# Optimization experiments

Hardware: AMD Instinct MI355X
Metric: run time of the kernel (lower is better)

## Reference

```python
import jax, jax.numpy as jnp
import numpy as np


def setup_inputs() -> dict:
    key = jax.random.key(0)
    ks = jax.random.split(key, 8)
    B = 65536
    x = jax.random.normal(ks[0], (B, 784), dtype=jnp.float32)
    conv_w = jnp.ones((3, 3), dtype=jnp.float32)  # Parameter(ones((3,3)))
    # Linear layers stored as (in, out) weight + (out,) bias
    def lin(k, fin, fout):
        kw, kb = jax.random.split(k)
        bound = 1.0 / np.sqrt(fin)
        W = jax.random.uniform(kw, (fin, fout), minval=-bound, maxval=bound, dtype=jnp.float32)
        b = jax.random.uniform(kb, (fout,), minval=-bound, maxval=bound, dtype=jnp.float32)
        return W, b
    W1, b1 = lin(ks[1], 26 * 26, 500)
    W2, b2 = lin(ks[2], 500, 200)
    W3, b3 = lin(ks[3], 200, 10)
    return {"x": x, "conv_w": conv_w, "W1": W1, "b1": b1,
            "W2": W2, "b2": b2, "W3": W3, "b3": b3}


def reference(x, conv_w, W1, b1, W2, b2, W3, b3):
    B = x.shape[0]
    img = x.reshape(B, 1, 28, 28)  # NCHW, single channel
    kern = conv_w.reshape(1, 1, 3, 3)  # OIHW
    # valid 2D cross-correlation == torch tensordot sliding-window loop
    conv = jax.lax.conv_general_dilated(
        img, kern, window_strides=(1, 1), padding='VALID',
        dimension_numbers=('NCHW', 'OIHW', 'NCHW'))  # (B,1,26,26)
    h = conv.reshape(B, 26 * 26)
    h = jax.nn.relu(h @ W1 + b1)
    h = jax.nn.relu(h @ W2 + b2)
    return h @ W3 + b3  # (B, 10) logits
```

## Files before the change

### kernel.cpp

```cpp
#include <hip/hip_runtime.h>
#include <hip/hip_bf16.h>
#include <stdint.h>

typedef __bf16 bf16x8 __attribute__((ext_vector_type(8)));
typedef float  f32x4  __attribute__((ext_vector_type(4)));


#define KT1 25
#define NF1 32
#define KT2 16
#define NF2 16
#define KT3 8

__global__ void prep_w1(const float* __restrict__ W1, const float* __restrict__ cw,
                        __bf16* __restrict__ w1s) {
  int gid  = blockIdx.x * 256 + threadIdx.x;
  int lane = gid & 63;
  int slot = gid >> 6;
  int t = slot >> 5;
  int f = slot & 31;
  int kbase = t * 32 + ((lane >> 4) << 3);
  int n = f * 16 + (lane & 15);
  float c[9];
#pragma unroll
  for (int i = 0; i < 9; ++i) c[i] = cw[i];
  bf16x8 v;
#pragma unroll
  for (int e = 0; e < 8; ++e) {
    int k = kbase + e;
    float acc = 0.f;
    if (k < 784 && n < 500) {
      int pi = k / 28, pj = k % 28;
#pragma unroll
      for (int dr = 0; dr < 3; ++dr) {
        int r = pi - dr;
        if (r < 0 || r >= 26) continue;
#pragma unroll
        for (int dc = 0; dc < 3; ++dc) {
          int cc = pj - dc;
          if (cc < 0 || cc >= 26) continue;
          acc += c[dr * 3 + dc] * W1[(size_t)(r * 26 + cc) * 500 + n];
        }
      }
    }
    v[e] = (__bf16)acc;
  }
  *(bf16x8*)(w1s + (size_t)(slot * 64 + lane) * 8) = v;
}

__global__ void prep_w2(const float* __restrict__ W2, __bf16* __restrict__ w2s) {
  int gid  = blockIdx.x * 256 + threadIdx.x;
  int lane = gid & 63;
  int slot = gid >> 6;
  int t = slot >> 4;
  int f = slot & 15;
  int kbase = t * 32 + ((lane >> 4) << 3);
  int n = f * 16 + (lane & 15);
  bf16x8 v;
#pragma unroll
  for (int e = 0; e < 8; ++e) {
    int k = kbase + e;
    float val = (k < 500 && n < 200) ? W2[(size_t)k * 200 + n] : 0.f;
    v[e] = (__bf16)val;
  }
  *(bf16x8*)(w2s + (size_t)(slot * 64 + lane) * 8) = v;
}

__global__ void prep_w3(const float* __restrict__ W3, __bf16* __restrict__ w3s) {
  int gid  = blockIdx.x * 256 + threadIdx.x;
  int lane = gid & 63;
  int t    = gid >> 6;
  int kbase = t * 32 + ((lane >> 4) << 3);
  int n = lane & 15;
  bf16x8 v;
#pragma unroll
  for (int e = 0; e < 8; ++e) {
    int k = kbase + e;
    float val = (k < 200 && n < 10) ? W3[(size_t)k * 10 + n] : 0.f;
    v[e] = (__bf16)val;
  }
  *(bf16x8*)(w3s + (size_t)(t * 64 + lane) * 8) = v;
}

__global__ __launch_bounds__(256, 2) void mlp_fused(
    const float* __restrict__ x,
    const __bf16* __restrict__ w1s, const __bf16* __restrict__ w2s,
    const __bf16* __restrict__ w3s,
    const float* __restrict__ b1, const float* __restrict__ b2,
    const float* __restrict__ b3,
    float* __restrict__ out)
{
  __shared__ __align__(16) char xsm[2 * 4096];
  __shared__ __align__(16) char h1[64 * 1024];
  __shared__ float sb1[512];
  __shared__ float sb2[256];

  const int tid  = threadIdx.x;
  const int lane = tid & 63;
  const int w    = tid >> 6;
  const int lrow = lane & 15;
  const int lgrp = lane >> 4;
  const int brow = blockIdx.x * 64;
  const int xr   = tid >> 2;
  const int xq   = tid & 3;

  sb1[tid]       = (tid < 500) ? b1[tid] : 0.f;
  sb1[tid + 256] = (tid + 256 < 500) ? b1[tid + 256] : 0.f;
  sb2[tid]       = (tid < 200) ? b2[tid] : 0.f;

  const f32x4 FZ = {0.f, 0.f, 0.f, 0.f};

  f32x4 acc1[4][8];
#pragma unroll
  for (int m = 0; m < 4; ++m)
#pragma unroll
    for (int f = 0; f < 8; ++f) acc1[m][f] = FZ;

  const bf16x8* w1p   = (const bf16x8*)w1s + ((size_t)(w * 8) * 64 + lane);
  const float*  xbase = x + (size_t)(brow + xr) * 784;
  const int     xswz  = (xq ^ (xr & 3)) << 4;
  const int     xoff  = xr * 64 + xswz;

  auto gload = [&](int t, f32x4 (&g)[2]) {
    int gk = t * 32 + xq * 8;
    if (gk > 776) gk = 776;
    const float* p = xbase + gk;
    g[0] = *(const f32x4*)p;
    g[1] = *(const f32x4*)(p + 4);
  };
  auto cwrite = [&](f32x4 (&g)[2], int bw) {
    bf16x8 v;
#pragma unroll
    for (int e = 0; e < 4; ++e) { v[e] = (__bf16)g[0][e]; v[e + 4] = (__bf16)g[1][e]; }
    *(bf16x8*)(xsm + bw + xoff) = v;
  };

  f32x4  grA[2], grB[2];
  bf16x8 bA[8], bB[8];

  auto body1 = [&](int t, bf16x8 (&bc)[8], bf16x8 (&bn)[8],
                   f32x4 (&gc)[2], f32x4 (&gl)[2], int bufR, int bufW) {
    bf16x8 afr[4];
#pragma unroll
    for (int m = 0; m < 4; ++m) {
      int r = m * 16 + lrow;
      afr[m] = *(const bf16x8*)(xsm + bufR + r * 64 + ((lgrp ^ (r & 3)) << 4));
    }
#pragma unroll
    for (int f = 0; f < 8; ++f) bn[f] = w1p[(size_t)((t + 1) * NF1 + f) * 64];
    gload(t + 2 > 24 ? 24 : t + 2, gl);
    cwrite(gc, bufW);

    __builtin_amdgcn_s_setprio(1);
#pragma unroll
    for (int f = 0; f < 8; ++f)
#pragma unroll
      for (int m = 0; m < 4; ++m)
        acc1[m][f] = __builtin_amdgcn_mfma_f32_16x16x32_bf16(afr[m], bc[f], acc1[m][f], 0, 0, 0);
    __builtin_amdgcn_s_setprio(0);

    asm volatile("s_waitcnt lgkmcnt(0)\n\ts_barrier" ::: "memory");
  };

  gload(0, grA);
#pragma unroll
  for (int f = 0; f < 8; ++f) bA[f] = w1p[(size_t)f * 64];
  gload(1, grB);
  cwrite(grA, 0);
  asm volatile("s_waitcnt lgkmcnt(0)\n\ts_barrier" ::: "memory");

  for (int t = 0; t < 24; t += 2) {
    body1(t,     bA, bB, grB, grA, 0,    4096);
    body1(t + 1, bB, bA, grA, grB, 4096, 0);
  }
  {
    bf16x8 afr[4];
#pragma unroll
    for (int m = 0; m < 4; ++m) {
      int r = m * 16 + lrow;
      afr[m] = *(const bf16x8*)(xsm + r * 64 + ((lgrp ^ (r & 3)) << 4));
    }
    __builtin_amdgcn_s_setprio(1);
#pragma unroll
    for (int f = 0; f < 8; ++f)
#pragma unroll
      for (int m = 0; m < 4; ++m)
        acc1[m][f] = __builtin_amdgcn_mfma_f32_16x16x32_bf16(afr[m], bA[f], acc1[m][f], 0, 0, 0);
    __builtin_amdgcn_s_setprio(0);
  }

#pragma unroll
  for (int m = 0; m < 4; ++m) {
#pragma unroll
    for (int f = 0; f < 8; ++f) {
      int col = w * 128 + f * 16 + lrow;
      float bias = sb1[col];
#pragma unroll
      for (int r = 0; r < 4; ++r) {
        int row = m * 16 + lgrp * 4 + r;
        float v = fmaxf(acc1[m][f][r] + bias, 0.f);
        int off = row * 1024 + ((col * 2) ^ ((row & 7) << 4));
        *(__bf16*)(h1 + off) = (__bf16)v;
      }
    }
  }
  __syncthreads();

  f32x4 acc2[4][4];
#pragma unroll
  for (int m = 0; m < 4; ++m)
#pragma unroll
    for (int f = 0; f < 4; ++f) acc2[m][f] = FZ;

  const bf16x8* w2p = (const bf16x8*)w2s + ((size_t)(w * 4) * 64 + lane);

  bf16x8 b2a[4], b2b[4];
#pragma unroll
  for (int f = 0; f < 4; ++f) b2a[f] = w2p[(size_t)f * 64];

  for (int t = 0; t < KT2; t += 2) {
#pragma unroll
    for (int f = 0; f < 4; ++f) b2b[f] = w2p[(size_t)((t + 1) * NF2 + f) * 64];
    {
      bf16x8 a2[4];
#pragma unroll
      for (int m = 0; m < 4; ++m) {
        int row = m * 16 + lrow;
        int off = row * 1024 + ((t * 64 + lgrp * 16) ^ ((row & 7) << 4));
        a2[m] = *(const bf16x8*)(h1 + off);
      }
      __builtin_amdgcn_s_setprio(1);
#pragma unroll
      for (int f = 0; f < 4; ++f)
#pragma unroll
        for (int m = 0; m < 4; ++m)
          acc2[m][f] = __builtin_amdgcn_mfma_f32_16x16x32_bf16(a2[m], b2a[f], acc2[m][f], 0, 0, 0);
      __builtin_amdgcn_s_setprio(0);
    }
#pragma unroll
    for (int f = 0; f < 4; ++f) b2a[f] = w2p[(size_t)((t + 2) * NF2 + f) * 64];
    {
      bf16x8 a2[4];
#pragma unroll
      for (int m = 0; m < 4; ++m) {
        int row = m * 16 + lrow;
        int off = row * 1024 + (((t + 1) * 64 + lgrp * 16) ^ ((row & 7) << 4));
        a2[m] = *(const bf16x8*)(h1 + off);
      }
      __builtin_amdgcn_s_setprio(1);
#pragma unroll
      for (int f = 0; f < 4; ++f)
#pragma unroll
        for (int m = 0; m < 4; ++m)
          acc2[m][f] = __builtin_amdgcn_mfma_f32_16x16x32_bf16(a2[m], b2b[f], acc2[m][f], 0, 0, 0);
      __builtin_amdgcn_s_setprio(0);
    }
  }

  __syncthreads();

#pragma unroll
  for (int m = 0; m < 4; ++m) {
#pragma unroll
    for (int f = 0; f < 4; ++f) {
      int col = w * 64 + f * 16 + lrow;
      float bias = sb2[col];
#pragma unroll
      for (int r = 0; r < 4; ++r) {
        int row = m * 16 + lgrp * 4 + r;
        float v = fmaxf(acc2[m][f][r] + bias, 0.f);
        int off = row * 512 + ((col * 2) ^ ((row & 7) << 4));
        *(__bf16*)(h1 + off) = (__bf16)v;
      }
    }
  }
  __syncthreads();

  {
    f32x4 a3 = FZ;
    const bf16x8* w3p = (const bf16x8*)w3s + lane;
#pragma unroll
    for (int t = 0; t < KT3; ++t) {
      int row = w * 16 + lrow;
      int off = row * 512 + ((t * 64 + lgrp * 16) ^ ((row & 7) << 4));
      bf16x8 a = *(const bf16x8*)(h1 + off);
      a3 = __builtin_amdgcn_mfma_f32_16x16x32_bf16(a, w3p[(size_t)t * 64], a3, 0, 0, 0);
    }
    if (lrow < 10) {
      float bias = b3[lrow];
#pragma unroll
      for (int r = 0; r < 4; ++r)
        out[(size_t)(brow + w * 16 + lgrp * 4 + r) * 10 + lrow] = a3[r] + bias;
    }
  }
}

extern "C" void kernel_launch(void* const* d_in, const int* in_sizes, int n_in,
                              void* d_out, int out_size, void* d_ws, size_t ws_size,
                              hipStream_t stream) {
  const float* x  = (const float*)d_in[0];
  const float* cw = (const float*)d_in[1];
  const float* W1 = (const float*)d_in[2];
  const float* b1 = (const float*)d_in[3];
  const float* W2 = (const float*)d_in[4];
  const float* b2 = (const float*)d_in[5];
  const float* W3 = (const float*)d_in[6];
  const float* b3 = (const float*)d_in[7];
  float* out = (float*)d_out;

  __bf16* w1s = (__bf16*)d_ws;
  __bf16* w2s = w1s + (size_t)KT1 * NF1 * 64 * 8;
  __bf16* w3s = w2s + (size_t)KT2 * NF2 * 64 * 8;

  prep_w1<<<200, 256, 0, stream>>>(W1, cw, w1s);
  prep_w2<<<64, 256, 0, stream>>>(W2, w2s);
  prep_w3<<<2, 256, 0, stream>>>(W3, w3s);

  mlp_fused<<<65536 / 64, 256, 0, stream>>>(x, w1s, w2s, w3s, b1, b2, b3, out);
}
```

Baseline: 93.04 us.

## Stage four x K-tiles per barrier and alias x buffer with h1 LDS

Restructures the layer-1 pipeline so each stage loads four 32-wide K-tiles of x into registers, writes them as a 16KB bf16 LDS block, and double-buffers those blocks. A barrier is now needed only once per four tiles instead of once per tile, which cuts synchronisation cost and gives each global load more time to arrive. The x staging buffer is aliased onto the h1 activation buffer, so total LDS use drops from 72KB to 64KB plus biases. The cost is more registers holding in-flight loads, which may hurt occupancy at launch bounds of 2 blocks. The W2 prefetch is also moved ahead of the layer-1 epilogue.

```diff
diff --git a/kernel.cpp b/kernel.cpp
--- a/kernel.cpp
+++ b/kernel.cpp
@@ -90,8 +90,7 @@
     const float* __restrict__ b3,
     float* __restrict__ out)
 {
-  __shared__ __align__(16) char xsm[2 * 4096];
-  __shared__ __align__(16) char h1[64 * 1024];
+  __shared__ __align__(16) char smem[64 * 1024];
   __shared__ float sb1[512];
   __shared__ float sb2[256];
 
@@ -118,39 +117,45 @@
 
   const bf16x8* w1p   = (const bf16x8*)w1s + ((size_t)(w * 8) * 64 + lane);
   const float*  xbase = x + (size_t)(brow + xr) * 784;
-  const int     xswz  = (xq ^ (xr & 3)) << 4;
-  const int     xoff  = xr * 64 + xswz;
-
-  auto gload = [&](int t, f32x4 (&g)[2]) {
-    int gk = t * 32 + xq * 8;
-    if (gk > 776) gk = 776;
-    const float* p = xbase + gk;
-    g[0] = *(const f32x4*)p;
-    g[1] = *(const f32x4*)(p + 4);
+  const int     xoff  = xr * 64 + ((xq ^ (xr & 3)) << 4);
+
+  f32x4 g[4][2];
+
+  auto gload4 = [&](int s) {
+#pragma unroll
+    for (int j = 0; j < 4; ++j) {
+      int tile = s * 4 + j;
+      if (tile > 24) tile = 24;
+      int gk = tile * 32 + xq * 8;
+      if (gk > 776) gk = 776;
+      const float* p = xbase + gk;
+      g[j][0] = *(const f32x4*)p;
+      g[j][1] = *(const f32x4*)(p + 4);
+    }
   };
-  auto cwrite = [&](f32x4 (&g)[2], int bw) {
-    bf16x8 v;
-#pragma unroll
-    for (int e = 0; e < 4; ++e) { v[e] = (__bf16)g[0][e]; v[e + 4] = (__bf16)g[1][e]; }
-    *(bf16x8*)(xsm + bw + xoff) = v;
+  auto cwrite4 = [&](int buf) {
+#pragma unroll
+    for (int j = 0; j < 4; ++j) {
+      bf16x8 v;
+#pragma unroll
+      for (int e = 0; e < 4; ++e) { v[e] = (__bf16)g[j][0][e]; v[e + 4] = (__bf16)g[j][1][e]; }
+      *(bf16x8*)(smem + buf * 16384 + j * 4096 + xoff) = v;
+    }
   };
 
-  f32x4  grA[2], grB[2];
   bf16x8 bA[8], bB[8];
 
-  auto body1 = [&](int t, bf16x8 (&bc)[8], bf16x8 (&bn)[8],
-                   f32x4 (&gc)[2], f32x4 (&gl)[2], int bufR, int bufW) {
+  auto ktile = [&](int tile, int rb, int slot, bf16x8 (&bc)[8], bf16x8 (&bn)[8], bool pf) {
     bf16x8 afr[4];
 #pragma unroll
     for (int m = 0; m < 4; ++m) {
       int r = m * 16 + lrow;
-      afr[m] = *(const bf16x8*)(xsm + bufR + r * 64 + ((lgrp ^ (r & 3)) << 4));
-    }
-#pragma unroll
-    for (int f = 0; f < 8; ++f) bn[f] = w1p[(size_t)((t + 1) * NF1 + f) * 64];
-    gload(t + 2 > 24 ? 24 : t + 2, gl);
-    cwrite(gc, bufW);
-
+      afr[m] = *(const bf16x8*)(smem + rb + slot * 4096 + r * 64 + ((lgrp ^ (r & 3)) << 4));
+    }
+    if (pf) {
+#pragma unroll
+      for (int f = 0; f < 8; ++f) bn[f] = w1p[(size_t)((tile + 1) * NF1 + f) * 64];
+    }
     __builtin_amdgcn_s_setprio(1);
 #pragma unroll
     for (int f = 0; f < 8; ++f)
@@ -158,36 +163,33 @@
       for (int m = 0; m < 4; ++m)
         acc1[m][f] = __builtin_amdgcn_mfma_f32_16x16x32_bf16(afr[m], bc[f], acc1[m][f], 0, 0, 0);
     __builtin_amdgcn_s_setprio(0);
-
+  };
+
+  gload4(0);
+#pragma unroll
+  for (int f = 0; f < 8; ++f) bA[f] = w1p[(size_t)f * 64];
+  cwrite4(0);
+  asm volatile("s_waitcnt lgkmcnt(0)\n\ts_barrier" ::: "memory");
+
+  for (int s = 0; s < 6; ++s) {
+    int rb = (s & 1) * 16384;
+    gload4(s + 1);
+    int t0 = s * 4;
+    ktile(t0 + 0, rb, 0, bA, bB, true);
+    ktile(t0 + 1, rb, 1, bB, bA, true);
+    ktile(t0 + 2, rb, 2, bA, bB, true);
+    ktile(t0 + 3, rb, 3, bB, bA, true);
+    cwrite4((s + 1) & 1);
     asm volatile("s_waitcnt lgkmcnt(0)\n\ts_barrier" ::: "memory");
-  };
-
-  gload(0, grA);
-#pragma unroll
-  for (int f = 0; f < 8; ++f) bA[f] = w1p[(size_t)f * 64];
-  gload(1, grB);
-  cwrite(grA, 0);
+  }
+  ktile(24, 0, 0, bA, bB, false);
+
+  const bf16x8* w2p = (const bf16x8*)w2s + ((size_t)(w * 4) * 64 + lane);
+  bf16x8 b2a[4], b2b[4];
+#pragma unroll
+  for (int f = 0; f < 4; ++f) b2a[f] = w2p[(size_t)f * 64];
+
   asm volatile("s_waitcnt lgkmcnt(0)\n\ts_barrier" ::: "memory");
-
-  for (int t = 0; t < 24; t += 2) {
-    body1(t,     bA, bB, grB, grA, 0,    4096);
-    body1(t + 1, bB, bA, grA, grB, 4096, 0);
-  }
-  {
-    bf16x8 afr[4];
-#pragma unroll
-    for (int m = 0; m < 4; ++m) {
-      int r = m * 16 + lrow;
-      afr[m] = *(const bf16x8*)(xsm + r * 64 + ((lgrp ^ (r & 3)) << 4));
-    }
-    __builtin_amdgcn_s_setprio(1);
-#pragma unroll
-    for (int f = 0; f < 8; ++f)
-#pragma unroll
-      for (int m = 0; m < 4; ++m)
-        acc1[m][f] = __builtin_amdgcn_mfma_f32_16x16x32_bf16(afr[m], bA[f], acc1[m][f], 0, 0, 0);
-    __builtin_amdgcn_s_setprio(0);
-  }
 
 #pragma unroll
   for (int m = 0; m < 4; ++m) {
@@ -200,7 +202,7 @@
         int row = m * 16 + lgrp * 4 + r;
         float v = fmaxf(acc1[m][f][r] + bias, 0.f);
         int off = row * 1024 + ((col * 2) ^ ((row & 7) << 4));
-        *(__bf16*)(h1 + off) = (__bf16)v;
+        *(__bf16*)(smem + off) = (__bf16)v;
       }
     }
   }
@@ -211,12 +213,6 @@
   for (int m = 0; m < 4; ++m)
 #pragma unroll
     for (int f = 0; f < 4; ++f) acc2[m][f] = FZ;
-
-  const bf16x8* w2p = (const bf16x8*)w2s + ((size_t)(w * 4) * 64 + lane);
-
-  bf16x8 b2a[4], b2b[4];
-#pragma unroll
-  for (int f = 0; f < 4; ++f) b2a[f] = w2p[(size_t)f * 64];
 
   for (int t = 0; t < KT2; t += 2) {
 #pragma unroll
@@ -227,7 +223,7 @@
       for (int m = 0; m < 4; ++m) {
         int row = m * 16 + lrow;
         int off = row * 1024 + ((t * 64 + lgrp * 16) ^ ((row & 7) << 4));
-        a2[m] = *(const bf16x8*)(h1 + off);
+        a2[m] = *(const bf16x8*)(smem + off);
       }
       __builtin_amdgcn_s_setprio(1);
 #pragma unroll
@@ -245,7 +241,7 @@
       for (int m = 0; m < 4; ++m) {
         int row = m * 16 + lrow;
         int off = row * 1024 + (((t + 1) * 64 + lgrp * 16) ^ ((row & 7) << 4));
-        a2[m] = *(const bf16x8*)(h1 + off);
+        a2[m] = *(const bf16x8*)(smem + off);
       }
       __builtin_amdgcn_s_setprio(1);
 #pragma unroll
@@ -270,7 +266,7 @@
         int row = m * 16 + lgrp * 4 + r;
         float v = fmaxf(acc2[m][f][r] + bias, 0.f);
         int off = row * 512 + ((col * 2) ^ ((row & 7) << 4));
-        *(__bf16*)(h1 + off) = (__bf16)v;
+        *(__bf16*)(smem + off) = (__bf16)v;
       }
     }
   }
@@ -283,7 +279,7 @@
     for (int t = 0; t < KT3; ++t) {
       int row = w * 16 + lrow;
       int off = row * 512 + ((t * 64 + lgrp * 16) ^ ((row & 7) << 4));
-      bf16x8 a = *(const bf16x8*)(h1 + off);
+      bf16x8 a = *(const bf16x8*)(smem + off);
       a3 = __builtin_amdgcn_mfma_f32_16x16x32_bf16(a, w3p[(size_t)t * 64], a3, 0, 0, 0);
     }
     if (lrow < 10) {
```

After: 99.66 us. +7.1%, slower.
